# Optimization experiments

Measured on AMD Instinct MI355X. Metric: run time of the kernel, lower is better.

## Reference

```python
import jax, jax.numpy as jnp
import numpy as np

B, T, H, LATENT, COND = 256, 256, 512, 64, 6
IN0 = 3 + H + 4  # lstm layer-0 input size


def _ln(x, g, b, eps=1e-5):
    m = x.mean(-1, keepdims=True)
    v = ((x - m) ** 2).mean(-1, keepdims=True)
    return (x - m) / jnp.sqrt(v + eps) * g + b


def setup_inputs() -> dict:
    key = jax.random.key(0)
    ks = jax.random.split(key, 24)
    p = lambda k, shape: (jax.random.normal(k, shape) * 0.02).astype(jnp.float32)
    inp = {
        'start': jax.random.uniform(ks[0], (B, 2), dtype=jnp.float32),
        'end': jax.random.uniform(ks[1], (B, 2), dtype=jnp.float32),
        'z': jax.random.normal(ks[2], (B, LATENT), dtype=jnp.float32),
        # condition encoder: Linear(6+latent->H), LN, Linear(H->H), LN
        'ce_w1': p(ks[3], (H, COND + LATENT)), 'ce_b1': jnp.zeros((H,), jnp.float32),
        'ce_g1': jnp.ones((H,), jnp.float32), 'ce_be1': jnp.zeros((H,), jnp.float32),
        'ce_w2': p(ks[4], (H, H)), 'ce_b2': jnp.zeros((H,), jnp.float32),
        'ce_g2': jnp.ones((H,), jnp.float32), 'ce_be2': jnp.zeros((H,), jnp.float32),
        # 2-layer LSTM (torch gate order i,f,g,o)
        'Wih0': p(ks[5], (4 * H, IN0)), 'Whh0': p(ks[6], (4 * H, H)),
        'bih0': jnp.zeros((4 * H,), jnp.float32), 'bhh0': jnp.zeros((4 * H,), jnp.float32),
        'Wih1': p(ks[7], (4 * H, H)), 'Whh1': p(ks[8], (4 * H, H)),
        'bih1': jnp.zeros((4 * H,), jnp.float32), 'bhh1': jnp.zeros((4 * H,), jnp.float32),
        # output head: Linear(H->H//2), LeakyReLU, Linear(H//2->3)
        'ow1': p(ks[9], (H // 2, H)), 'ob1': jnp.zeros((H // 2,), jnp.float32),
        'ow2': p(ks[10], (3, H // 2)), 'ob2': jnp.zeros((3,), jnp.float32),
        'init_in': jnp.zeros((1, 1, 3), jnp.float32),
        'max_len': T,
    }
    return inp


def _cell(x, h, c, Wih, Whh, bih, bhh):
    g = x @ Wih.T + bih + h @ Whh.T + bhh
    i, f, gg, o = jnp.split(g, 4, axis=-1)
    c2 = jax.nn.sigmoid(f) * c + jax.nn.sigmoid(i) * jnp.tanh(gg)
    h2 = jax.nn.sigmoid(o) * jnp.tanh(c2)
    return h2, c2


def reference(start, end, z, ce_w1, ce_b1, ce_g1, ce_be1, ce_w2, ce_b2, ce_g2, ce_be2,
              Wih0, Whh0, bih0, bhh0, Wih1, Whh1, bih1, bhh1,
              ow1, ob1, ow2, ob2, init_in, max_len):
    b = start.shape[0]
    hd = Whh0.shape[1]
    # condition vector
    diff = end - start
    dist = jnp.sqrt((diff ** 2).sum(-1, keepdims=True) + 1e-8)
    ang = jnp.arctan2(diff[:, 1:2], diff[:, 0:1])
    ci = jnp.concatenate([start, end, dist, ang, z], axis=-1)
    x = jax.nn.leaky_relu(_ln(ci @ ce_w1.T + ce_b1, ce_g1, ce_be1), 0.2)
    cond = jax.nn.leaky_relu(_ln(x @ ce_w2.T + ce_b2, ce_g2, ce_be2), 0.2)

    h0 = jnp.zeros((2, b, hd), start.dtype)
    c0 = jnp.zeros((2, b, hd), start.dtype)
    cur_in0 = jnp.broadcast_to(init_in.reshape(1, 3), (b, 3))

    def step(carry, _):
        h, c, cur_in, pos = carry
        rem = end - pos
        rd = jnp.sqrt((rem ** 2).sum(-1, keepdims=True) + 1e-8)
        ra = jnp.arctan2(rem[:, 1:2], rem[:, 0:1])
        xin = jnp.concatenate([cur_in, cond, rem, rd, ra], axis=-1)  # (B, 3+H+4)
        h1, c1 = _cell(xin, h[0], c[0], Wih0, Whh0, bih0, bhh0)
        h2, c2 = _cell(h1, h[1], c[1], Wih1, Whh1, bih1, bhh1)
        o = jax.nn.leaky_relu(h2 @ ow1.T + ob1, 0.2) @ ow2.T + ob2  # (B, 3)
        out = jnp.concatenate([o[:, :2], jax.nn.softplus(o[:, 2:3]) + 0.001], axis=-1)
        pos = pos + out[:, :2]
        return (jnp.stack([h1, h2]), jnp.stack([c1, c2]), out, pos), out

    _, outs = jax.lax.scan(step, (h0, c0, cur_in0, start), None, length=max_len)
    outputs = jnp.transpose(outs, (1, 0, 2))  # (B, T, 3)
    lengths = jnp.full((b,), max_len, dtype=jnp.int32)
    return outputs, lengths
```

## Files before the change

### kernel.cpp

```cpp
#include <hip/hip_runtime.h>
#include <math.h>

#define BB 256
#define TT 256
#define HH 512
#define G4 2048
#define IN0_ 519

typedef __bf16 bf16x8 __attribute__((ext_vector_type(8)));
typedef float  f32x4  __attribute__((ext_vector_type(4)));
typedef unsigned short ushort;
typedef unsigned long long u64;

__device__ __forceinline__ float sigf(float x) { return 1.0f / (1.0f + expf(-x)); }
__device__ __forceinline__ float leaky(float x) { return x > 0.f ? x : 0.2f * x; }

__device__ __forceinline__ ushort f2b(float x) {
    union { float f; unsigned int u; } v; v.f = x;
    unsigned int r = v.u + 0x7fffu + ((v.u >> 16) & 1u);
    return (ushort)(r >> 16);
}

__device__ __forceinline__ float block_sum(float v, float* red, int tid) {
    red[tid] = v; __syncthreads();
    for (int s = 128; s > 0; s >>= 1) {
        if (tid < s) red[tid] += red[tid + s];
        __syncthreads();
    }
    float r = red[0];
    __syncthreads();
    return r;
}

#define SWZB(row, bo) ((bo) ^ (((((row) ^ ((bo) >> 6)) & 7)) << 4))
#define LDA(Abuf, lr_, lk_, kt_) \
    (*(const bf16x8*)&Abuf[((lr_) * 1024 + SWZB((lr_), (kt_)*64 + (lk_)*16)) >> 1])

__device__ __forceinline__ void stageA(ushort* dst, const ushort* src, int m0, int tid) {
    int row = tid >> 4;
    int lanebo = (tid & 15) * 64;
    const ushort* sp = src + (size_t)(m0 + row) * HH;
    #pragma unroll
    for (int j = 0; j < 4; j++) {
        int b2 = lanebo + j * 16;
        uint4 v = *(const uint4*)(sp + (b2 >> 1));
        *(uint4*)&dst[((row * 1024) + SWZB(row, b2)) >> 1] = v;
    }
}

__device__ __forceinline__ void stage_at(ushort* dst, const ushort* src, int m0, int tid) {
    int row = tid >> 4;
    int lane = tid & 15;
    const u64* sp = (const u64*)(src + (size_t)(m0 + row) * HH) + lane * 8;
    #pragma unroll
    for (int j = 0; j < 8; j++) {
        u64 v = __hip_atomic_load(sp + j, __ATOMIC_RELAXED, __HIP_MEMORY_SCOPE_AGENT);
        int b2 = lane * 64 + j * 8;
        *(u64*)&dst[((row * 1024) + SWZB(row, b2)) >> 1] = v;
    }
}

__device__ __forceinline__ void team_barrier(unsigned* cnt, unsigned target) {
    __syncthreads();
    if (threadIdx.x == 0) {
        __hip_atomic_fetch_add(cnt, 1u, __ATOMIC_RELAXED, __HIP_MEMORY_SCOPE_AGENT);
        while (__hip_atomic_load(cnt, __ATOMIC_RELAXED, __HIP_MEMORY_SCOPE_AGENT) < target)
            __builtin_amdgcn_s_sleep(2);
    }
    __syncthreads();
}

#define SHIDX(jgt, kt, l_) ((((size_t)(jgt) * 16 + (kt)) * 64 + (l_)) * 8)

__global__ __launch_bounds__(256) void prep_all(
    const float* __restrict__ Whh0, const float* __restrict__ Wih1,
    const float* __restrict__ Whh1, const float* __restrict__ Wih0,
    const float* __restrict__ ow1,
    ushort* __restrict__ w0s, ushort* __restrict__ w1s,
    ushort* __restrict__ w2s, ushort* __restrict__ wi0s,
    ushort* __restrict__ ow1s, float* __restrict__ Wf)
{
    size_t idx = (size_t)blockIdx.x * 256 + threadIdx.x;
    const size_t M = 1u << 20;
    if (idx < 4 * M) {
        int m = (int)(idx >> 20);
        unsigned i = (unsigned)(idx & (M - 1));
        int e = i & 7, ll = (i >> 3) & 63, kt = (i >> 9) & 15, jgt = i >> 13;
        int jg = jgt * 16 + (ll & 15);
        int k  = kt * 32 + ((ll >> 4) << 3) + e;
        float v;
        if (m == 0)      v = Whh0[(size_t)jg * 512 + k];
        else if (m == 1) v = Wih1[(size_t)jg * 512 + k];
        else if (m == 2) v = Whh1[(size_t)jg * 512 + k];
        else             v = Wih0[(size_t)jg * IN0_ + 3 + k];
        ushort* dst = (m == 0) ? w0s : (m == 1) ? w1s : (m == 2) ? w2s : wi0s;
        dst[i] = f2b(v);
    } else if (idx < 4 * M + 131072) {
        unsigned i = (unsigned)(idx - 4 * M);
        int e = i & 7, ll = (i >> 3) & 63, kt = (i >> 9) & 15, jgt = i >> 13;
        int jg = jgt * 16 + (ll & 15);
        int k  = kt * 32 + ((ll >> 4) << 3) + e;
        ow1s[i] = f2b(ow1[(size_t)jg * 512 + k]);
    } else if (idx < 4 * M + 131072 + 2048) {
        int jrow = (int)(idx - (4 * M + 131072));
        const int fc[7] = {0, 1, 2, 515, 516, 517, 518};
        #pragma unroll
        for (int f = 0; f < 7; f++) Wf[jrow * 8 + f] = Wih0[(size_t)jrow * IN0_ + fc[f]];
        Wf[jrow * 8 + 7] = 0.f;
    }
}

__global__ __launch_bounds__(256) void cond_encoder(
    const float* __restrict__ start, const float* __restrict__ end,
    const float* __restrict__ z,
    const float* __restrict__ w1, const float* __restrict__ b1,
    const float* __restrict__ g1, const float* __restrict__ be1,
    const float* __restrict__ w2, const float* __restrict__ b2,
    const float* __restrict__ g2, const float* __restrict__ be2,
    ushort* __restrict__ condb)
{
    __shared__ float ci[70];
    __shared__ float xr[512];
    __shared__ float red[256];
    int b = blockIdx.x, tid = threadIdx.x;
    if (tid == 0) {
        float sx = start[2*b], sy = start[2*b+1];
        float ex = end[2*b],   ey = end[2*b+1];
        float dx = ex - sx, dy = ey - sy;
        ci[0]=sx; ci[1]=sy; ci[2]=ex; ci[3]=ey;
        ci[4]=sqrtf(dx*dx + dy*dy + 1e-8f);
        ci[5]=atan2f(dy, dx);
    }
    if (tid < 64) ci[6+tid] = z[b*64 + tid];
    __syncthreads();

    float pre0 = b1[tid], pre1 = b1[tid+256];
    {
        const float* r0 = w1 + (size_t)tid*70;
        const float* r1 = w1 + (size_t)(tid+256)*70;
        for (int k = 0; k < 70; k++) { float c = ci[k]; pre0 += c*r0[k]; pre1 += c*r1[k]; }
    }
    float m = block_sum(pre0+pre1, red, tid) * (1.f/512.f);
    float d0 = pre0-m, d1 = pre1-m;
    float v = block_sum(d0*d0 + d1*d1, red, tid) * (1.f/512.f);
    float rstd = rsqrtf(v + 1e-5f);
    xr[tid]     = leaky(d0*rstd*g1[tid]     + be1[tid]);
    xr[tid+256] = leaky(d1*rstd*g1[tid+256] + be1[tid+256]);
    __syncthreads();

    float q0 = b2[tid], q1 = b2[tid+256];
    {
        const float4* r0 = (const float4*)(w2 + (size_t)tid*512);
        const float4* r1 = (const float4*)(w2 + (size_t)(tid+256)*512);
        const float4* xv4 = (const float4*)xr;
        for (int q = 0; q < 128; q++) {
            float4 xv = xv4[q];
            float4 wa = r0[q], wb = r1[q];
            q0 += xv.x*wa.x + xv.y*wa.y + xv.z*wa.z + xv.w*wa.w;
            q1 += xv.x*wb.x + xv.y*wb.y + xv.z*wb.z + xv.w*wb.w;
        }
    }
    m = block_sum(q0+q1, red, tid) * (1.f/512.f);
    d0 = q0-m; d1 = q1-m;
    v = block_sum(d0*d0 + d1*d1, red, tid) * (1.f/512.f);
    rstd = rsqrtf(v + 1e-5f);
    condb[(size_t)b*512 + tid]     = f2b(leaky(d0*rstd*g2[tid]     + be2[tid]));
    condb[(size_t)b*512 + tid+256] = f2b(leaky(d1*rstd*g2[tid+256] + be2[tid+256]));
}

__global__ __launch_bounds__(256) void gs0_mfma(
    const ushort* __restrict__ condb, const ushort* __restrict__ wi0s,
    const float* __restrict__ bih0, const float* __restrict__ bhh0,
    float* __restrict__ gs0)
{
    __shared__ ushort A1[16*512];
    int tid = threadIdx.x;
    int bt = blockIdx.x >> 4, ct2 = blockIdx.x & 15;
    int m0 = bt*16, hc0 = ct2*32;
    int wid = tid >> 6, l = tid & 63, lr = l & 15, lk = l >> 4;
    stageA(A1, condb, m0, tid);
    __syncthreads();
    int jgb = wid*512 + hc0;
    float bv0 = bih0[jgb+lr]    + bhh0[jgb+lr];
    float bv1 = bih0[jgb+16+lr] + bhh0[jgb+16+lr];
    f32x4 a0, a1;
    #pragma unroll
    for (int r = 0; r < 4; r++) { a0[r] = bv0; a1[r] = bv1; }
    int jgt = jgb >> 4;
    #pragma unroll
    for (int kt = 0; kt < 16; kt++) {
        bf16x8 av = LDA(A1, lr, lk, kt);
        bf16x8 b0 = *(const bf16x8*)&wi0s[SHIDX(jgt,   kt, l)];
        bf16x8 b1 = *(const bf16x8*)&wi0s[SHIDX(jgt+1, kt, l)];
        a0 = __builtin_amdgcn_mfma_f32_16x16x32_bf16(av, b0, a0, 0, 0, 0);
        a1 = __builtin_amdgcn_mfma_f32_16x16x32_bf16(av, b1, a1, 0, 0, 0);
    }
    #pragma unroll
    for (int r = 0; r < 4; r++) {
        gs0[(size_t)(m0 + lk*4 + r)*G4 + jgb + lr]      = a0[r];
        gs0[(size_t)(m0 + lk*4 + r)*G4 + jgb + 16 + lr] = a1[r];
    }
}

__global__ __launch_bounds__(256, 1) void rollout(
    const ushort* __restrict__ w0s, const ushort* __restrict__ w1s,
    const ushort* __restrict__ w2s, const ushort* __restrict__ ow1s,
    const float* __restrict__ gs0, const float* __restrict__ WfG,
    const float* __restrict__ bih1, const float* __restrict__ bhh1,
    const float* __restrict__ ob1, const float* __restrict__ ow2,
    const float* __restrict__ ob2,
    const float* __restrict__ start, const float* __restrict__ endp,
    const float* __restrict__ init_in, const int* __restrict__ max_len,
    ushort* __restrict__ h0A, ushort* __restrict__ h0B,
    ushort* __restrict__ h1A, ushort* __restrict__ h1B,
    float* __restrict__ outp, unsigned* __restrict__ bar)
{
    __shared__ ushort A1[16*512];
    __shared__ ushort A2[16*512];
    __shared__ float scratch[16*257];
    __shared__ float WfS[4*32*9];
    __shared__ ushort hstage[512];
    __shared__ float feats[16][8];
    __shared__ float posS[16][2], endS[16][2], osumS[16][3];

    int tid = threadIdx.x;
    int blk = blockIdx.x;
    int xcd = blk & 7, wi = blk >> 3;
    int ct = xcd*2 + (wi & 1);
    int bt = wi >> 1;
    int m0 = bt*16, hc0 = ct*32;
    int wid = tid >> 6, l = tid & 63, lr = l & 15, lk = l >> 4;
    unsigned* cnt = bar + bt*16;

    for (int i = tid; i < 4*32*8; i += 256) {
        int g = i >> 8, rem = i & 255, col = rem >> 3, f = rem & 7;
        WfS[(g*32+col)*9 + f] = WfG[(size_t)(g*512 + hc0 + col)*8 + f];
    }
    if (tid < 16) {
        int b = m0 + tid;
        posS[tid][0] = start[2*b]; posS[tid][1] = start[2*b+1];
        endS[tid][0] = endp[2*b];  endS[tid][1] = endp[2*b+1];
        if (ct == 0) outp[(size_t)BB*TT*3 + b] = (float)max_len[0];
    }
    __syncthreads();
    if (tid < 16) {
        float rx = endS[tid][0]-posS[tid][0], ry = endS[tid][1]-posS[tid][1];
        feats[tid][0]=init_in[0]; feats[tid][1]=init_in[1]; feats[tid][2]=init_in[2];
        feats[tid][3]=rx; feats[tid][4]=ry;
        feats[tid][5]=sqrtf(rx*rx+ry*ry+1e-8f);
        feats[tid][6]=atan2f(ry,rx);
    }

    f32x4 gsr[2]; float b1r[2]; float ob1r[4];
    #pragma unroll
    for (int nt = 0; nt < 2; nt++) {
        int jg = wid*512 + hc0 + nt*16 + lr;
        #pragma unroll
        for (int r = 0; r < 4; r++) gsr[nt][r] = gs0[(size_t)(m0 + lk*4 + r)*G4 + jg];
        b1r[nt] = bih1[jg] + bhh1[jg];
    }
    #pragma unroll
    for (int q = 0; q < 4; q++) ob1r[q] = ob1[wid*64 + q*16 + lr];

    if (tid < 128) {
        int row = tid >> 3, cc = (tid & 7) * 4;
        __hip_atomic_store((u64*)&h0A[(size_t)(m0+row)*HH + hc0 + cc], 0ull,
                           __ATOMIC_RELAXED, __HIP_MEMORY_SCOPE_AGENT);
        __hip_atomic_store((u64*)&h1A[(size_t)(m0+row)*HH + hc0 + cc], 0ull,
                           __ATOMIC_RELAXED, __HIP_MEMORY_SCOPE_AGENT);
    }
    float c00 = 0.f, c01 = 0.f, c10 = 0.f, c11 = 0.f;

    unsigned bseq = 1;
    team_barrier(cnt, bseq*16u);

    int jgt0 = wid*32 + ct*2;
    #pragma unroll 1
    for (int t = 0; t < TT; t++) {
        const ushort* h0in  = (t & 1) ? h0B : h0A;
        ushort*       h0out = (t & 1) ? h0A : h0B;
        const ushort* h1in  = (t & 1) ? h1B : h1A;
        ushort*       h1out = (t & 1) ? h1A : h1B;

        stage_at(A1, h0in, m0, tid);
        __syncthreads();
        {
            f32x4 a0 = gsr[0], a1 = gsr[1];
            #pragma unroll
            for (int kt = 0; kt < 16; kt++) {
                bf16x8 av  = LDA(A1, lr, lk, kt);
                bf16x8 b0  = *(const bf16x8*)&w0s[SHIDX(jgt0,   kt, l)];
                bf16x8 b1v = *(const bf16x8*)&w0s[SHIDX(jgt0+1, kt, l)];
                a0 = __builtin_amdgcn_mfma_f32_16x16x32_bf16(av, b0,  a0, 0, 0, 0);
                a1 = __builtin_amdgcn_mfma_f32_16x16x32_bf16(av, b1v, a1, 0, 0, 0);
            }
            #pragma unroll
            for (int r = 0; r < 4; r++) {
                scratch[(wid*16 + lk*4 + r)*33 + lr]      = a0[r];
                scratch[(wid*16 + lk*4 + r)*33 + 16 + lr] = a1[r];
            }
        }
        __syncthreads();
        #pragma unroll
        for (int s = 0; s < 2; s++) {
            int cell = tid + s*256;
            int row = cell >> 5, col = cell & 31;
            float gv[4];
            #pragma unroll
            for (int g = 0; g < 4; g++) {
                float v = scratch[(g*16 + row)*33 + col];
                const float* wf = &WfS[(g*32 + col)*9];
                #pragma unroll
                for (int f = 0; f < 7; f++) v += feats[row][f] * wf[f];
                gv[g] = v;
            }
            float cold = s ? c01 : c00;
            float cn = sigf(gv[1])*cold + sigf(gv[0])*tanhf(gv[2]);
            if (s) c01 = cn; else c00 = cn;
            hstage[cell] = f2b(sigf(gv[3])*tanhf(cn));
        }
        __syncthreads();
        if (tid < 128) {
            int row = tid >> 3, cc = (tid & 7) * 4;
            u64 v = *(const u64*)&hstage[row*32 + cc];
            __hip_atomic_store((u64*)&h0out[(size_t)(m0+row)*HH + hc0 + cc], v,
                               __ATOMIC_RELAXED, __HIP_MEMORY_SCOPE_AGENT);
        }
        bseq++; team_barrier(cnt, bseq*16u);

        stage_at(A1, h0out, m0, tid);
        stage_at(A2, h1in,  m0, tid);
        __syncthreads();
        {
            f32x4 a0, a1;
            #pragma unroll
            for (int r = 0; r < 4; r++) { a0[r] = b1r[0]; a1[r] = b1r[1]; }
            #pragma unroll
            for (int kt = 0; kt < 16; kt++) {
                bf16x8 av  = LDA(A1, lr, lk, kt);
                bf16x8 b0  = *(const bf16x8*)&w1s[SHIDX(jgt0,   kt, l)];
                bf16x8 b1v = *(const bf16x8*)&w1s[SHIDX(jgt0+1, kt, l)];
                a0 = __builtin_amdgcn_mfma_f32_16x16x32_bf16(av, b0,  a0, 0, 0, 0);
                a1 = __builtin_amdgcn_mfma_f32_16x16x32_bf16(av, b1v, a1, 0, 0, 0);
            }
            #pragma unroll
            for (int kt = 0; kt < 16; kt++) {
                bf16x8 av  = LDA(A2, lr, lk, kt);
                bf16x8 b0  = *(const bf16x8*)&w2s[SHIDX(jgt0,   kt, l)];
                bf16x8 b1v = *(const bf16x8*)&w2s[SHIDX(jgt0+1, kt, l)];
                a0 = __builtin_amdgcn_mfma_f32_16x16x32_bf16(av, b0,  a0, 0, 0, 0);
                a1 = __builtin_amdgcn_mfma_f32_16x16x32_bf16(av, b1v, a1, 0, 0, 0);
            }
            #pragma unroll
            for (int r = 0; r < 4; r++) {
                scratch[(wid*16 + lk*4 + r)*33 + lr]      = a0[r];
                scratch[(wid*16 + lk*4 + r)*33 + 16 + lr] = a1[r];
            }
        }
        __syncthreads();
        #pragma unroll
        for (int s = 0; s < 2; s++) {
            int cell = tid + s*256;
            int row = cell >> 5, col = cell & 31;
            float gi = scratch[(0*16+row)*33 + col];
            float gf = scratch[(1*16+row)*33 + col];
            float gg = scratch[(2*16+row)*33 + col];
            float go = scratch[(3*16+row)*33 + col];
            float cold = s ? c11 : c10;
            float cn = sigf(gf)*cold + sigf(gi)*tanhf(gg);
            if (s) c11 = cn; else c10 = cn;
            hstage[cell] = f2b(sigf(go)*tanhf(cn));
        }
        __syncthreads();
        if (tid < 128) {
            int row = tid >> 3, cc = (tid & 7) * 4;
            u64 v = *(const u64*)&hstage[row*32 + cc];
            __hip_atomic_store((u64*)&h1out[(size_t)(m0+row)*HH + hc0 + cc], v,
                               __ATOMIC_RELAXED, __HIP_MEMORY_SCOPE_AGENT);
        }
        bseq++; team_barrier(cnt, bseq*16u);

        stage_at(A1, h1out, m0, tid);
        __syncthreads();
        {
            f32x4 hacc[4];
            #pragma unroll
            for (int q = 0; q < 4; q++) {
                #pragma unroll
                for (int r = 0; r < 4; r++) hacc[q][r] = ob1r[q];
            }
            #pragma unroll
            for (int kt = 0; kt < 16; kt++) {
                bf16x8 av = LDA(A1, lr, lk, kt);
                #pragma unroll
                for (int q = 0; q < 4; q++) {
                    bf16x8 bv = *(const bf16x8*)&ow1s[SHIDX(wid*4 + q, kt, l)];
                    hacc[q] = __builtin_amdgcn_mfma_f32_16x16x32_bf16(av, bv, hacc[q], 0, 0, 0);
                }
            }
            #pragma unroll
            for (int q = 0; q < 4; q++)
                #pragma unroll
                for (int r = 0; r < 4; r++)
                    scratch[(lk*4 + r)*257 + wid*64 + q*16 + lr] = leaky(hacc[q][r]);
        }
        __syncthreads();
        if (tid < 48) {
            int row = tid & 15, rr = tid >> 4;
            const float* w2r = ow2 + rr*256;
            float sum = 0.f;
            for (int kk = 0; kk < 256; kk++) {
                int k = (kk + row*16) & 255;
                sum += scratch[row*257 + k] * w2r[k];
            }
            osumS[row][rr] = sum + ob2[rr];
        }
        __syncthreads();
        if (tid < 16) {
            int row = tid;
            float o0 = osumS[row][0], o1 = osumS[row][1], o2 = osumS[row][2];
            float sp = (o2 > 20.f ? o2 : log1pf(expf(o2))) + 0.001f;
            posS[row][0] += o0; posS[row][1] += o1;
            if (ct == 0) {
                float* op = outp + ((size_t)(m0+row)*TT + t)*3;
                op[0] = o0; op[1] = o1; op[2] = sp;
            }
            float rx = endS[row][0]-posS[row][0], ry = endS[row][1]-posS[row][1];
            feats[row][0]=o0; feats[row][1]=o1; feats[row][2]=sp;
            feats[row][3]=rx; feats[row][4]=ry;
            feats[row][5]=sqrtf(rx*rx+ry*ry+1e-8f);
            feats[row][6]=atan2f(ry,rx);
        }
        __syncthreads();
    }
}

extern "C" void kernel_launch(void* const* d_in, const int* in_sizes, int n_in,
                              void* d_out, int out_size, void* d_ws, size_t ws_size,
                              hipStream_t stream)
{
    const float* start  = (const float*)d_in[0];
    const float* end    = (const float*)d_in[1];
    const float* z      = (const float*)d_in[2];
    const float* ce_w1  = (const float*)d_in[3];
    const float* ce_b1  = (const float*)d_in[4];
    const float* ce_g1  = (const float*)d_in[5];
    const float* ce_be1 = (const float*)d_in[6];
    const float* ce_w2  = (const float*)d_in[7];
    const float* ce_b2  = (const float*)d_in[8];
    const float* ce_g2  = (const float*)d_in[9];
    const float* ce_be2 = (const float*)d_in[10];
    const float* Wih0   = (const float*)d_in[11];
    const float* Whh0   = (const float*)d_in[12];
    const float* bih0   = (const float*)d_in[13];
    const float* bhh0   = (const float*)d_in[14];
    const float* Wih1   = (const float*)d_in[15];
    const float* Whh1   = (const float*)d_in[16];
    const float* bih1   = (const float*)d_in[17];
    const float* bhh1   = (const float*)d_in[18];
    const float* ow1    = (const float*)d_in[19];
    const float* ob1    = (const float*)d_in[20];
    const float* ow2    = (const float*)d_in[21];
    const float* ob2    = (const float*)d_in[22];
    const float* init_in= (const float*)d_in[23];
    const int*   max_len= (const int*)d_in[24];

    float* out = (float*)d_out;
    float* ws  = (float*)d_ws;
    size_t off = 0;
    float* gs0  = ws + off; off += (size_t)BB*G4;
    float* WfG  = ws + off; off += (size_t)G4*8;
    unsigned* bar = (unsigned*)(ws + off); off += 256;
    ushort* us = (ushort*)(ws + off);
    size_t uo = 0;
    ushort* w0s  = us + uo; uo += (size_t)G4*HH;
    ushort* w1s  = us + uo; uo += (size_t)G4*HH;
    ushort* w2s  = us + uo; uo += (size_t)G4*HH;
    ushort* wi0s = us + uo; uo += (size_t)G4*HH;
    ushort* ow1s = us + uo; uo += (size_t)256*HH;
    ushort* condb= us + uo; uo += (size_t)BB*HH;
    ushort* h0A  = us + uo; uo += (size_t)BB*HH;
    ushort* h0B  = us + uo; uo += (size_t)BB*HH;
    ushort* h1A  = us + uo; uo += (size_t)BB*HH;
    ushort* h1B  = us + uo; uo += (size_t)BB*HH;

    hipMemsetAsync(bar, 0, 256*sizeof(unsigned), stream);
    {
        size_t total = (size_t)4*1048576 + 131072 + 2048;
        prep_all<<<dim3((unsigned)((total + 255)/256)), dim3(256), 0, stream>>>(
            Whh0, Wih1, Whh1, Wih0, ow1, w0s, w1s, w2s, wi0s, ow1s, WfG);
    }
    cond_encoder<<<dim3(BB), dim3(256), 0, stream>>>(
        start, end, z, ce_w1, ce_b1, ce_g1, ce_be1, ce_w2, ce_b2, ce_g2, ce_be2, condb);
    gs0_mfma<<<dim3(256), dim3(256), 0, stream>>>(condb, wi0s, bih0, bhh0, gs0);

    rollout<<<dim3(256), dim3(256), 0, stream>>>(
        w0s, w1s, w2s, ow1s, gs0, WfG, bih1, bhh1, ob1, ow2, ob2,
        start, end, init_in, max_len, h0A, h0B, h1A, h1B, out, bar);
}
```

Baseline: 14.71 ms.

## Keep LSTM hidden states resident in LDS and overlap h0 fetch with Whh1 MFMAs

The h0 and h1 tiles now live in persistent LDS buffers across time steps. This drops the per-step restaging of h0in before layer 0 and of h1in before layer 1, and the global h buffers go from double- to single-buffered. Layer 1 first runs the Whh1·h1 MFMAs from LDS while the atomic loads of the new h0 from global are in flight, then writes h0 to LDS and runs the Wih1 part. Single-buffered globals depend on the existing team barriers ordering reads before the next writes, and holding the loaded values across the MFMAs adds register pressure.

```diff
diff --git a/kernel.cpp b/kernel.cpp
--- a/kernel.cpp
+++ b/kernel.cpp
@@ -48,16 +48,17 @@
     }
 }
 
-__device__ __forceinline__ void stage_at(ushort* dst, const ushort* src, int m0, int tid) {
-    int row = tid >> 4;
-    int lane = tid & 15;
+__device__ __forceinline__ void stage_batched(ushort* dst, const ushort* src, int m0, int tid) {
+    int row = tid >> 4, lane = tid & 15;
     const u64* sp = (const u64*)(src + (size_t)(m0 + row) * HH) + lane * 8;
-    #pragma unroll
-    for (int j = 0; j < 8; j++) {
-        u64 v = __hip_atomic_load(sp + j, __ATOMIC_RELAXED, __HIP_MEMORY_SCOPE_AGENT);
-        int b2 = lane * 64 + j * 8;
-        *(u64*)&dst[((row * 1024) + SWZB(row, b2)) >> 1] = v;
-    }
+    u64 v[8];
+    #pragma unroll
+    for (int j = 0; j < 8; j++)
+        v[j] = __hip_atomic_load(sp + j, __ATOMIC_RELAXED, __HIP_MEMORY_SCOPE_AGENT);
+    int base = row * 1024, lb = lane * 64;
+    #pragma unroll
+    for (int j = 0; j < 8; j++)
+        *(u64*)&dst[(base + SWZB(row, lb + j * 8)) >> 1] = v[j];
 }
 
 __device__ __forceinline__ void team_barrier(unsigned* cnt, unsigned target) {
@@ -211,12 +212,11 @@
     const float* __restrict__ ob2,
     const float* __restrict__ start, const float* __restrict__ endp,
     const float* __restrict__ init_in, const int* __restrict__ max_len,
-    ushort* __restrict__ h0A, ushort* __restrict__ h0B,
-    ushort* __restrict__ h1A, ushort* __restrict__ h1B,
+    ushort* __restrict__ h0g, ushort* __restrict__ h1g,
     float* __restrict__ outp, unsigned* __restrict__ bar)
 {
-    __shared__ ushort A1[16*512];
-    __shared__ ushort A2[16*512];
+    __shared__ ushort A_h0[16*512];
+    __shared__ ushort A_h1[16*512];
     __shared__ float scratch[16*257];
     __shared__ float WfS[4*32*9];
     __shared__ ushort hstage[512];
@@ -236,6 +236,7 @@
         int g = i >> 8, rem = i & 255, col = rem >> 3, f = rem & 7;
         WfS[(g*32+col)*9 + f] = WfG[(size_t)(g*512 + hc0 + col)*8 + f];
     }
+    for (int i = tid; i < 16*512; i += 256) { A_h0[i] = 0; A_h1[i] = 0; }
     if (tid < 16) {
         int b = m0 + tid;
         posS[tid][0] = start[2*b]; posS[tid][1] = start[2*b+1];
@@ -261,34 +262,19 @@
     }
     #pragma unroll
     for (int q = 0; q < 4; q++) ob1r[q] = ob1[wid*64 + q*16 + lr];
-
-    if (tid < 128) {
-        int row = tid >> 3, cc = (tid & 7) * 4;
-        __hip_atomic_store((u64*)&h0A[(size_t)(m0+row)*HH + hc0 + cc], 0ull,
-                           __ATOMIC_RELAXED, __HIP_MEMORY_SCOPE_AGENT);
-        __hip_atomic_store((u64*)&h1A[(size_t)(m0+row)*HH + hc0 + cc], 0ull,
-                           __ATOMIC_RELAXED, __HIP_MEMORY_SCOPE_AGENT);
-    }
+    __syncthreads();
+
     float c00 = 0.f, c01 = 0.f, c10 = 0.f, c11 = 0.f;
-
-    unsigned bseq = 1;
-    team_barrier(cnt, bseq*16u);
-
+    unsigned bseq = 0;
     int jgt0 = wid*32 + ct*2;
+
     #pragma unroll 1
     for (int t = 0; t < TT; t++) {
-        const ushort* h0in  = (t & 1) ? h0B : h0A;
-        ushort*       h0out = (t & 1) ? h0A : h0B;
-        const ushort* h1in  = (t & 1) ? h1B : h1A;
-        ushort*       h1out = (t & 1) ? h1A : h1B;
-
-        stage_at(A1, h0in, m0, tid);
-        __syncthreads();
         {
             f32x4 a0 = gsr[0], a1 = gsr[1];
             #pragma unroll
             for (int kt = 0; kt < 16; kt++) {
-                bf16x8 av  = LDA(A1, lr, lk, kt);
+                bf16x8 av  = LDA(A_h0, lr, lk, kt);
                 bf16x8 b0  = *(const bf16x8*)&w0s[SHIDX(jgt0,   kt, l)];
                 bf16x8 b1v = *(const bf16x8*)&w0s[SHIDX(jgt0+1, kt, l)];
                 a0 = __builtin_amdgcn_mfma_f32_16x16x32_bf16(av, b0,  a0, 0, 0, 0);
@@ -323,39 +309,49 @@
         if (tid < 128) {
             int row = tid >> 3, cc = (tid & 7) * 4;
             u64 v = *(const u64*)&hstage[row*32 + cc];
-            __hip_atomic_store((u64*)&h0out[(size_t)(m0+row)*HH + hc0 + cc], v,
+            __hip_atomic_store((u64*)&h0g[(size_t)(m0+row)*HH + hc0 + cc], v,
                                __ATOMIC_RELAXED, __HIP_MEMORY_SCOPE_AGENT);
         }
         bseq++; team_barrier(cnt, bseq*16u);
 
-        stage_at(A1, h0out, m0, tid);
-        stage_at(A2, h1in,  m0, tid);
-        __syncthreads();
+        int srow = tid >> 4, slane = tid & 15;
+        u64 hv[8];
         {
-            f32x4 a0, a1;
-            #pragma unroll
-            for (int r = 0; r < 4; r++) { a0[r] = b1r[0]; a1[r] = b1r[1]; }
-            #pragma unroll
-            for (int kt = 0; kt < 16; kt++) {
-                bf16x8 av  = LDA(A1, lr, lk, kt);
-                bf16x8 b0  = *(const bf16x8*)&w1s[SHIDX(jgt0,   kt, l)];
-                bf16x8 b1v = *(const bf16x8*)&w1s[SHIDX(jgt0+1, kt, l)];
-                a0 = __builtin_amdgcn_mfma_f32_16x16x32_bf16(av, b0,  a0, 0, 0, 0);
-                a1 = __builtin_amdgcn_mfma_f32_16x16x32_bf16(av, b1v, a1, 0, 0, 0);
-            }
-            #pragma unroll
-            for (int kt = 0; kt < 16; kt++) {
-                bf16x8 av  = LDA(A2, lr, lk, kt);
-                bf16x8 b0  = *(const bf16x8*)&w2s[SHIDX(jgt0,   kt, l)];
-                bf16x8 b1v = *(const bf16x8*)&w2s[SHIDX(jgt0+1, kt, l)];
-                a0 = __builtin_amdgcn_mfma_f32_16x16x32_bf16(av, b0,  a0, 0, 0, 0);
-                a1 = __builtin_amdgcn_mfma_f32_16x16x32_bf16(av, b1v, a1, 0, 0, 0);
-            }
-            #pragma unroll
-            for (int r = 0; r < 4; r++) {
-                scratch[(wid*16 + lk*4 + r)*33 + lr]      = a0[r];
-                scratch[(wid*16 + lk*4 + r)*33 + 16 + lr] = a1[r];
-            }
+            const u64* sp = (const u64*)(h0g + (size_t)(m0 + srow) * HH) + slane * 8;
+            #pragma unroll
+            for (int j = 0; j < 8; j++)
+                hv[j] = __hip_atomic_load(sp + j, __ATOMIC_RELAXED, __HIP_MEMORY_SCOPE_AGENT);
+        }
+        f32x4 a0, a1;
+        #pragma unroll
+        for (int r = 0; r < 4; r++) { a0[r] = b1r[0]; a1[r] = b1r[1]; }
+        #pragma unroll
+        for (int kt = 0; kt < 16; kt++) {
+            bf16x8 av  = LDA(A_h1, lr, lk, kt);
+            bf16x8 b0  = *(const bf16x8*)&w2s[SHIDX(jgt0,   kt, l)];
+            bf16x8 b1v = *(const bf16x8*)&w2s[SHIDX(jgt0+1, kt, l)];
+            a0 = __builtin_amdgcn_mfma_f32_16x16x32_bf16(av, b0,  a0, 0, 0, 0);
+            a1 = __builtin_amdgcn_mfma_f32_16x16x32_bf16(av, b1v, a1, 0, 0, 0);
+        }
+        {
+            int base = srow * 1024, lb = slane * 64;
+            #pragma unroll
+            for (int j = 0; j < 8; j++)
+                *(u64*)&A_h0[(base + SWZB(srow, lb + j * 8)) >> 1] = hv[j];
+        }
+        __syncthreads();
+        #pragma unroll
+        for (int kt = 0; kt < 16; kt++) {
+            bf16x8 av  = LDA(A_h0, lr, lk, kt);
+            bf16x8 b0  = *(const bf16x8*)&w1s[SHIDX(jgt0,   kt, l)];
+            bf16x8 b1v = *(const bf16x8*)&w1s[SHIDX(jgt0+1, kt, l)];
+            a0 = __builtin_amdgcn_mfma_f32_16x16x32_bf16(av, b0,  a0, 0, 0, 0);
+            a1 = __builtin_amdgcn_mfma_f32_16x16x32_bf16(av, b1v, a1, 0, 0, 0);
+        }
+        #pragma unroll
+        for (int r = 0; r < 4; r++) {
+            scratch[(wid*16 + lk*4 + r)*33 + lr]      = a0[r];
+            scratch[(wid*16 + lk*4 + r)*33 + 16 + lr] = a1[r];
         }
         __syncthreads();
         #pragma unroll
@@ -375,12 +371,12 @@
         if (tid < 128) {
             int row = tid >> 3, cc = (tid & 7) * 4;
             u64 v = *(const u64*)&hstage[row*32 + cc];
-            __hip_atomic_store((u64*)&h1out[(size_t)(m0+row)*HH + hc0 + cc], v,
+            __hip_atomic_store((u64*)&h1g[(size_t)(m0+row)*HH + hc0 + cc], v,
                                __ATOMIC_RELAXED, __HIP_MEMORY_SCOPE_AGENT);
         }
         bseq++; team_barrier(cnt, bseq*16u);
 
-        stage_at(A1, h1out, m0, tid);
+        stage_batched(A_h1, h1g, m0, tid);
         __syncthreads();
         {
             f32x4 hacc[4];
@@ -391,7 +387,7 @@
             }
             #pragma unroll
             for (int kt = 0; kt < 16; kt++) {
-                bf16x8 av = LDA(A1, lr, lk, kt);
+                bf16x8 av = LDA(A_h1, lr, lk, kt);
                 #pragma unroll
                 for (int q = 0; q < 4; q++) {
                     bf16x8 bv = *(const bf16x8*)&ow1s[SHIDX(wid*4 + q, kt, l)];
@@ -479,10 +475,8 @@
     ushort* wi0s = us + uo; uo += (size_t)G4*HH;
     ushort* ow1s = us + uo; uo += (size_t)256*HH;
     ushort* condb= us + uo; uo += (size_t)BB*HH;
-    ushort* h0A  = us + uo; uo += (size_t)BB*HH;
-    ushort* h0B  = us + uo; uo += (size_t)BB*HH;
-    ushort* h1A  = us + uo; uo += (size_t)BB*HH;
-    ushort* h1B  = us + uo; uo += (size_t)BB*HH;
+    ushort* h0g  = us + uo; uo += (size_t)BB*HH;
+    ushort* h1g  = us + uo; uo += (size_t)BB*HH;
 
     hipMemsetAsync(bar, 0, 256*sizeof(unsigned), stream);
     {
@@ -496,5 +490,5 @@
 
     rollout<<<dim3(256), dim3(256), 0, stream>>>(
         w0s, w1s, w2s, ow1s, gs0, WfG, bih1, bhh1, ob1, ow2, ob2,
-        start, end, init_in, max_len, h0A, h0B, h1A, h1B, out, bar);
-}
+        start, end, init_in, max_len, h0g, h1g, out, bar);
+}
```

New measurement: 14.74 ms. No clear change (+0.2%).
